# Kernel optimization log

Measured on AMD Instinct MI355X. Metric: run time of the kernel, lower is better.

Reference implementation:

```python
import jax, jax.numpy as jnp
import numpy as np


def _get_rel_pos(q_size, k_size, rel_pos):
    # table length is assumed == 2*max(q,k)-1 (no interpolation path)
    q_coords = jnp.arange(q_size)[:, None] * max(k_size / q_size, 1.0)
    k_coords = jnp.arange(k_size)[None, :] * max(q_size / k_size, 1.0)
    rel = (q_coords - k_coords + (k_size - 1) * max(q_size / k_size, 1.0)).astype(jnp.int32)
    return rel_pos[rel]  # (q_size, k_size, head_dim)


def setup_inputs() -> dict:
    key = jax.random.key(0)
    ks = jax.random.split(key, 7)
    B, N, C = 8, 1024, 768
    s = 0.02
    return {
        "x": jax.random.normal(ks[0], (B, N, C), jnp.float32),
        "qkv_w": jax.random.normal(ks[1], (3 * C, C), jnp.float32) * s,
        "qkv_b": jax.random.normal(ks[2], (3 * C,), jnp.float32) * s,
        "proj_w": jax.random.normal(ks[3], (C, C), jnp.float32) * s,
        "proj_b": jax.random.normal(ks[4], (C,), jnp.float32) * s,
        "rel_pos_h": jax.random.normal(ks[5], (63, 64), jnp.float32) * s,
        "rel_pos_w": jax.random.normal(ks[6], (63, 64), jnp.float32) * s,
        "H": 32,
        "W": 32,
    }


def reference(x, qkv_w, qkv_b, proj_w, proj_b, rel_pos_h, rel_pos_w, H, W):
    B, N, C = x.shape
    hd = rel_pos_h.shape[-1]
    nh = C // hd
    scale = hd ** -0.5

    qkv = (x @ qkv_w.T + qkv_b).reshape(B, N, 3, nh, hd)
    q, k, v = [qkv[:, :, i].transpose(0, 2, 1, 3) for i in range(3)]  # (B, nh, N, hd)

    # decomposed relative position bias on the last H*W query/key tokens (here all of them)
    Rh = _get_rel_pos(H, H, rel_pos_h)  # (H, H, hd)
    Rw = _get_rel_pos(W, W, rel_pos_w)  # (W, W, hd)
    r_q = q.reshape(B * nh, H, W, hd)
    rel_h = jnp.einsum("bhwc,hkc->bhwk", r_q, Rh)  # (B*nh, H, W, H)
    rel_w = jnp.einsum("bhwc,wkc->bhwk", r_q, Rw)  # (B*nh, H, W, W)
    bias = (rel_h[..., :, None] + rel_w[..., None, :]).reshape(B, nh, N, N)

    scores = jnp.einsum("bhqd,bhkd->bhqk", q * scale, k) + bias
    attn = jax.nn.softmax(scores, axis=-1)
    out = jnp.einsum("bhqk,bhkd->bhqd", attn, v)  # (B, nh, N, hd)
    out = out.transpose(0, 2, 1, 3).reshape(B, N, C)
    out = out @ proj_w.T + proj_b

    pre_kv = jnp.stack([k.reshape(B * nh, N, hd), v.reshape(B * nh, N, hd)])
    return out, pre_kv
```

## Files before the change

kernel.cpp:

```cpp
#include <hip/hip_runtime.h>
#include <hip/hip_bf16.h>
#include <stdint.h>

typedef __attribute__((ext_vector_type(8))) short bf16x8;
typedef __attribute__((ext_vector_type(4))) float f32x4;

#define LOG2E 1.4426950408889634f

__device__ __forceinline__ float exp2_fast(float x) {
  float r; asm("v_exp_f32 %0, %1" : "=v"(r) : "v"(x)); return r;
}

__device__ __forceinline__ void gload_lds16(const void* g, void* l) {
  typedef __attribute__((address_space(1))) void gv_t;
  typedef __attribute__((address_space(3))) void lv_t;
  __builtin_amdgcn_global_load_lds((gv_t*)(uintptr_t)g,
                                   (lv_t*)(uint32_t)(uintptr_t)l, 16, 0, 0);
}

__global__ __launch_bounds__(256) void cvt_bf16(const float* __restrict__ src,
                                                __hip_bfloat16* __restrict__ dst, int n4) {
  int i = blockIdx.x * 256 + threadIdx.x;
  if (i < n4) {
    float4 f = ((const float4*)src)[i];
    union { ushort4 u; __hip_bfloat16 h[4]; } pk;
    pk.h[0] = __float2bfloat16(f.x);
    pk.h[1] = __float2bfloat16(f.y);
    pk.h[2] = __float2bfloat16(f.z);
    pk.h[3] = __float2bfloat16(f.w);
    ((ushort4*)dst)[i] = pk.u;
  }
}

__global__ __launch_bounds__(256) void cvt_bf16_pad(const float* __restrict__ src,
                                                    __hip_bfloat16* __restrict__ dst,
                                                    int n4src, int n4tot, float scale) {
  int i = blockIdx.x * 256 + threadIdx.x;
  if (i < n4tot) {
    float4 f = (i < n4src) ? ((const float4*)src)[i] : make_float4(0.f, 0.f, 0.f, 0.f);
    union { ushort4 u; __hip_bfloat16 h[4]; } pk;
    pk.h[0] = __float2bfloat16(f.x * scale);
    pk.h[1] = __float2bfloat16(f.y * scale);
    pk.h[2] = __float2bfloat16(f.z * scale);
    pk.h[3] = __float2bfloat16(f.w * scale);
    ((ushort4*)dst)[i] = pk.u;
  }
}

__device__ __forceinline__ void gemm_tile_compute(const __hip_bfloat16* __restrict__ A,
                                                  const __hip_bfloat16* __restrict__ Bm,
                                                  int K, int bm, int bn,
                                                  f32x4 acc[4][4], char* lbase) {
  const int tid = threadIdx.x;
  const int lane = tid & 63, w = tid >> 6;
  const int wr = w >> 1, wc = w & 1;
  const int rrow = lane & 15, g16 = lane >> 4;

  for (int k0 = 0; k0 < K; k0 += 32) {
    #pragma unroll
    for (int i = 0; i < 2; ++i) {
      int c = i * 4 + w;
      int b = c * 1024 + (lane << 4);
      int row = b >> 6;
      int cbs = ((b >> 4) & 3) ^ (row & 3);
      const char* ga = (const char*)(A + (size_t)(bm * 128 + row) * K + k0) + cbs * 16;
      gload_lds16(ga, lbase + c * 1024);
      const char* gb = (const char*)(Bm + (size_t)(bn * 128 + row) * K + k0) + cbs * 16;
      gload_lds16(gb, lbase + 8192 + c * 1024);
    }
    asm volatile("s_waitcnt vmcnt(0)" ::: "memory");
    __syncthreads();

    bf16x8 af[4], bfr[4];
    #pragma unroll
    for (int i = 0; i < 4; ++i) {
      int row = wr * 64 + i * 16 + rrow;
      af[i] = *(const bf16x8*)(lbase + row * 64 + ((g16 * 16) ^ ((row & 3) << 4)));
      int col = wc * 64 + i * 16 + rrow;
      bfr[i] = *(const bf16x8*)(lbase + 8192 + col * 64 + ((g16 * 16) ^ ((col & 3) << 4)));
    }
    __builtin_amdgcn_s_setprio(1);
    #pragma unroll
    for (int i = 0; i < 4; ++i)
      #pragma unroll
      for (int j = 0; j < 4; ++j)
        acc[i][j] = __builtin_amdgcn_mfma_f32_16x16x32_bf16(af[i], bfr[j], acc[i][j], 0, 0, 0);
    __builtin_amdgcn_s_setprio(0);
    __syncthreads();
  }
}

__global__ __launch_bounds__(256) void gemm_qkv_kernel(
    const __hip_bfloat16* __restrict__ xb, const __hip_bfloat16* __restrict__ wqkv,
    const float* __restrict__ qkv_b,
    __hip_bfloat16* __restrict__ Qws, __hip_bfloat16* __restrict__ Kws,
    __hip_bfloat16* __restrict__ Vws, float* __restrict__ prekv) {
  __shared__ char smem[16384];
  f32x4 acc[4][4];
  const f32x4 z4 = {0.f, 0.f, 0.f, 0.f};
  #pragma unroll
  for (int i = 0; i < 4; ++i)
    #pragma unroll
    for (int j = 0; j < 4; ++j) acc[i][j] = z4;

  const int bn = blockIdx.x, bm = blockIdx.y;
  gemm_tile_compute(xb, wqkv, 768, bm, bn, acc, smem);

  const int lane = threadIdx.x & 63, w = threadIdx.x >> 6;
  const int wr = w >> 1, wc = w & 1;
  const int col0 = lane & 15, g = lane >> 4;
  #pragma unroll
  for (int j = 0; j < 4; ++j) {
    int n = bn * 128 + wc * 64 + j * 16 + col0;
    float bias = qkv_b[n];
    int which = n / 768;
    int head = (n >> 6) % 12;
    int d = n & 63;
    #pragma unroll
    for (int i = 0; i < 4; ++i) {
      #pragma unroll
      for (int r = 0; r < 4; ++r) {
        int m = bm * 128 + wr * 64 + i * 16 + g * 4 + r;
        float v = acc[i][j][r] + bias;
        int b = m >> 10, t = m & 1023;
        size_t idx = ((size_t)(b * 12 + head) << 16) + (t << 6) + d;
        __hip_bfloat16 hv = __float2bfloat16(v);
        if (which == 0) {
          Qws[idx] = hv;
        } else if (which == 1) {
          Kws[idx] = hv; prekv[idx] = v;
        } else {
          Vws[idx] = hv; prekv[6291456 + idx] = v;
        }
      }
    }
  }
}

__global__ __launch_bounds__(256) void gemm_proj_kernel(
    const __hip_bfloat16* __restrict__ Ows, const __hip_bfloat16* __restrict__ wproj,
    const float* __restrict__ proj_b, float* __restrict__ out) {
  __shared__ char smem[16384];
  f32x4 acc[4][4];
  const f32x4 z4 = {0.f, 0.f, 0.f, 0.f};
  #pragma unroll
  for (int i = 0; i < 4; ++i)
    #pragma unroll
    for (int j = 0; j < 4; ++j) acc[i][j] = z4;

  const int bn = blockIdx.x, bm = blockIdx.y;
  gemm_tile_compute(Ows, wproj, 768, bm, bn, acc, smem);

  const int lane = threadIdx.x & 63, w = threadIdx.x >> 6;
  const int wr = w >> 1, wc = w & 1;
  const int col0 = lane & 15, g = lane >> 4;
  #pragma unroll
  for (int j = 0; j < 4; ++j) {
    int n = bn * 128 + wc * 64 + j * 16 + col0;
    float bias = proj_b[n];
    #pragma unroll
    for (int i = 0; i < 4; ++i) {
      #pragma unroll
      for (int r = 0; r < 4; ++r) {
        int m = bm * 128 + wr * 64 + i * 16 + g * 4 + r;
        out[(size_t)m * 768 + n] = acc[i][j][r] + bias;
      }
    }
  }
}

#define VSWZ(hd) ((((hd) ^ ((hd) >> 3)) & 7) << 4)
__global__ __launch_bounds__(256, 3) void flash_attn(
    const __hip_bfloat16* __restrict__ Qws, const __hip_bfloat16* __restrict__ Kws,
    const __hip_bfloat16* __restrict__ Vws, const __hip_bfloat16* __restrict__ rphb,
    const __hip_bfloat16* __restrict__ rpwb, __hip_bfloat16* __restrict__ Ows) {
  __shared__ alignas(16) char smem[49152];
  float* s_relh = (float*)smem;
  char*  s_kt   = smem + 16384;
  char*  s_vt   = smem + 24576;
  char*  s_pt   = smem + 32768;
  float* s_rw   = (float*)(smem + 32768);

  const int tid = threadIdx.x, lane = tid & 63, w = tid >> 6;
  const int g16 = lane >> 4, c16 = lane & 15;
  const int bid = blockIdx.x;
  const int qt = bid / 96, bh = bid - qt * 96;
  const int q0 = qt * 128;
  const int b = bh / 12, head = bh - b * 12;
  const size_t bhbase = (size_t)bh << 16;

  bf16x8 qf[2][2];
  {
    const __hip_bfloat16* qp = Qws + bhbase + (size_t)(q0 + w * 32 + c16) * 64 + g16 * 8;
    qf[0][0] = *(const bf16x8*)qp;
    qf[0][1] = *(const bf16x8*)(qp + 32);
    qf[1][0] = *(const bf16x8*)(qp + 16 * 64);
    qf[1][1] = *(const bf16x8*)(qp + 16 * 64 + 32);
  }

  const f32x4 z4 = {0.f, 0.f, 0.f, 0.f};

  {
    f32x4 gh[2][4], gw[2][4];
    #pragma unroll
    for (int mb = 0; mb < 2; ++mb)
      #pragma unroll
      for (int nf = 0; nf < 4; ++nf) { gh[mb][nf] = z4; gw[mb][nf] = z4; }
    #pragma unroll
    for (int kc = 0; kc < 2; ++kc) {
      #pragma unroll
      for (int nf = 0; nf < 4; ++nf) {
        int j = nf * 16 + c16;
        bf16x8 th = *(const bf16x8*)(rphb + j * 64 + kc * 32 + g16 * 8);
        bf16x8 tw = *(const bf16x8*)(rpwb + j * 64 + kc * 32 + g16 * 8);
        gh[0][nf] = __builtin_amdgcn_mfma_f32_16x16x32_bf16(qf[0][kc], th, gh[0][nf], 0, 0, 0);
        gh[1][nf] = __builtin_amdgcn_mfma_f32_16x16x32_bf16(qf[1][kc], th, gh[1][nf], 0, 0, 0);
        gw[0][nf] = __builtin_amdgcn_mfma_f32_16x16x32_bf16(qf[0][kc], tw, gw[0][nf], 0, 0, 0);
        gw[1][nf] = __builtin_amdgcn_mfma_f32_16x16x32_bf16(qf[1][kc], tw, gw[1][nf], 0, 0, 0);
      }
    }
    const int hq = (q0 >> 5) + w;
    #pragma unroll
    for (int mb = 0; mb < 2; ++mb) {
      #pragma unroll
      for (int nf = 0; nf < 4; ++nf) {
        int j = nf * 16 + c16;
        int khh = hq - j + 31;
        #pragma unroll
        for (int r = 0; r < 4; ++r) {
          int rowin = mb * 16 + g16 * 4 + r;
          int lrow = w * 32 + rowin;
          if (khh >= 0 && khh < 32) s_relh[lrow * 32 + khh] = gh[mb][nf][r];
          int kww = rowin - j + 31;
          if (kww >= 0 && kww < 32) s_rw[lrow * 32 + kww] = gw[mb][nf][r];
        }
      }
    }
  }
  asm volatile("s_waitcnt lgkmcnt(0)" ::: "memory");
  float rw0[2][4], rw1[2][4];
  #pragma unroll
  for (int rb = 0; rb < 2; ++rb)
    #pragma unroll
    for (int r = 0; r < 4; ++r) {
      int lrow = w * 32 + rb * 16 + g16 * 4 + r;
      rw0[rb][r] = s_rw[lrow * 32 + c16];
      rw1[rb][r] = s_rw[lrow * 32 + 16 + c16];
    }

  f32x4 o[2][4];
  float m_r[2][4], l_r[2][4];
  #pragma unroll
  for (int rb = 0; rb < 2; ++rb) {
    #pragma unroll
    for (int hf = 0; hf < 4; ++hf) o[rb][hf] = z4;
    #pragma unroll
    for (int r = 0; r < 4; ++r) { m_r[rb][r] = -1e30f; l_r[rb][r] = 0.f; }
  }

  const float SCALE2 = 0.125f * LOG2E;
  const int kp = tid >> 3;
  const int hd0 = (tid & 7) * 8;

  for (int kt0 = 0; kt0 < 1024; kt0 += 64) {
    #pragma unroll
    for (int i = 0; i < 2; ++i) {
      int c = w * 2 + i;
      int row = c * 8 + (lane >> 3);
      int cbs = (lane & 7) ^ (row & 7);
      const char* g = (const char*)(Kws + bhbase + (size_t)(kt0 + row) * 64) + cbs * 16;
      gload_lds16(g, s_kt + c * 1024);
    }
    asm volatile("" ::: "memory");
    const __hip_bfloat16* vr = Vws + bhbase + (size_t)(kt0 + 2 * kp) * 64 + hd0;
    bf16x8 va = *(const bf16x8*)vr;
    bf16x8 vb = *(const bf16x8*)(vr + 64);
    asm volatile("s_waitcnt vmcnt(2)" ::: "memory");
    __builtin_amdgcn_s_barrier();

    f32x4 s[2][4];
    #pragma unroll
    for (int rb = 0; rb < 2; ++rb)
      #pragma unroll
      for (int kf = 0; kf < 4; ++kf) s[rb][kf] = z4;
    __builtin_amdgcn_s_setprio(1);
    #pragma unroll
    for (int kc = 0; kc < 2; ++kc) {
      #pragma unroll
      for (int kf = 0; kf < 4; ++kf) {
        int key = kf * 16 + c16;
        int byte = key * 128 + (((kc * 32 + g16 * 8) * 2) ^ ((key & 7) << 4));
        bf16x8 kfr = *(const bf16x8*)(s_kt + byte);
        s[0][kf] = __builtin_amdgcn_mfma_f32_16x16x32_bf16(qf[0][kc], kfr, s[0][kf], 0, 0, 0);
        s[1][kf] = __builtin_amdgcn_mfma_f32_16x16x32_bf16(qf[1][kc], kfr, s[1][kf], 0, 0, 0);
      }
    }
    __builtin_amdgcn_s_setprio(0);

    asm volatile("s_waitcnt vmcnt(0)" ::: "memory");
    #pragma unroll
    for (int j = 0; j < 8; ++j) {
      int hd = hd0 + j;
      union { ushort2 u2; uint32_t u; } pk;
      pk.u2.x = (unsigned short)va[j];
      pk.u2.y = (unsigned short)vb[j];
      *(uint32_t*)(s_vt + hd * 128 + ((4 * kp) ^ VSWZ(hd))) = pk.u;
    }

    int kh0 = kt0 >> 5;
    f32x4 facv[2];
    #pragma unroll
    for (int rb = 0; rb < 2; ++rb) {
      float rh0[4], rh1[4];
      #pragma unroll
      for (int r = 0; r < 4; ++r) {
        int lrow = w * 32 + rb * 16 + g16 * 4 + r;
        float2 rh = *(const float2*)&s_relh[lrow * 32 + kh0];
        rh0[r] = rh.x; rh1[r] = rh.y;
      }
      #pragma unroll
      for (int kf = 0; kf < 4; ++kf)
        #pragma unroll
        for (int r = 0; r < 4; ++r)
          s[rb][kf][r] = fmaf(s[rb][kf][r], SCALE2,
                              ((kf >> 1) ? rh1[r] : rh0[r]) +
                              ((kf & 1) ? rw1[rb][r] : rw0[rb][r]));
      #pragma unroll
      for (int r = 0; r < 4; ++r) {
        float tm = fmaxf(fmaxf(s[rb][0][r], s[rb][1][r]), fmaxf(s[rb][2][r], s[rb][3][r]));
        tm = fmaxf(tm, __shfl_xor(tm, 1));
        tm = fmaxf(tm, __shfl_xor(tm, 2));
        tm = fmaxf(tm, __shfl_xor(tm, 4));
        tm = fmaxf(tm, __shfl_xor(tm, 8));
        float mold = m_r[rb][r];
        float mnew = fmaxf(mold, tm);
        float fac = exp2_fast(mold - mnew);
        m_r[rb][r] = mnew;
        facv[rb][r] = fac;
        float psum = 0.f;
        #pragma unroll
        for (int kf = 0; kf < 4; ++kf) {
          float p = exp2_fast(s[rb][kf][r] - mnew);
          s[rb][kf][r] = p;
          psum += p;
        }
        psum += __shfl_xor(psum, 1);
        psum += __shfl_xor(psum, 2);
        psum += __shfl_xor(psum, 4);
        psum += __shfl_xor(psum, 8);
        l_r[rb][r] = fmaf(l_r[rb][r], fac, psum);
      }
    }
    bool nr = (facv[0][0] == 1.f) & (facv[0][1] == 1.f) & (facv[0][2] == 1.f) &
              (facv[0][3] == 1.f) & (facv[1][0] == 1.f) & (facv[1][1] == 1.f) &
              (facv[1][2] == 1.f) & (facv[1][3] == 1.f);
    if (!__all(nr)) {
      #pragma unroll
      for (int rb = 0; rb < 2; ++rb)
        #pragma unroll
        for (int hf = 0; hf < 4; ++hf) o[rb][hf] *= facv[rb];
    }

    #pragma unroll
    for (int rb = 0; rb < 2; ++rb)
      #pragma unroll
      for (int kf = 0; kf < 4; ++kf) {
        int key = kf * 16 + c16;
        #pragma unroll
        for (int r = 0; r < 4; ++r) {
          int prow = rb * 16 + g16 * 4 + r;
          int byte = w * 4096 + prow * 128 + ((key * 2) ^ ((prow & 7) << 4));
          *(__hip_bfloat16*)(s_pt + byte) = __float2bfloat16(s[rb][kf][r]);
        }
      }

    asm volatile("s_waitcnt lgkmcnt(0)" ::: "memory");
    __builtin_amdgcn_s_barrier();

    __builtin_amdgcn_s_setprio(1);
    #pragma unroll
    for (int kc = 0; kc < 2; ++kc) {
      bf16x8 pf[2];
      #pragma unroll
      for (int rb = 0; rb < 2; ++rb) {
        int prow = rb * 16 + c16;
        int byte = w * 4096 + prow * 128 + (((kc * 32 + g16 * 8) * 2) ^ ((prow & 7) << 4));
        pf[rb] = *(const bf16x8*)(s_pt + byte);
      }
      #pragma unroll
      for (int hf = 0; hf < 4; ++hf) {
        int hd = hf * 16 + c16;
        int byte = hd * 128 + (((kc * 32 + g16 * 8) * 2) ^ VSWZ(hd));
        bf16x8 vf = *(const bf16x8*)(s_vt + byte);
        o[0][hf] = __builtin_amdgcn_mfma_f32_16x16x32_bf16(pf[0], vf, o[0][hf], 0, 0, 0);
        o[1][hf] = __builtin_amdgcn_mfma_f32_16x16x32_bf16(pf[1], vf, o[1][hf], 0, 0, 0);
      }
    }
    __builtin_amdgcn_s_setprio(0);
  }

  #pragma unroll
  for (int rb = 0; rb < 2; ++rb) {
    #pragma unroll
    for (int r = 0; r < 4; ++r) {
      int row = q0 + w * 32 + rb * 16 + g16 * 4 + r;
      float inv = 1.0f / l_r[rb][r];
      size_t base = ((size_t)b * 1024 + row) * 768 + head * 64;
      #pragma unroll
      for (int hf = 0; hf < 4; ++hf)
        Ows[base + hf * 16 + c16] = __float2bfloat16(o[rb][hf][r] * inv);
    }
  }
}

extern "C" void kernel_launch(void* const* d_in, const int* in_sizes, int n_in,
                              void* d_out, int out_size, void* d_ws, size_t ws_size,
                              hipStream_t stream) {
  const float* x      = (const float*)d_in[0];
  const float* qkv_w  = (const float*)d_in[1];
  const float* qkv_b  = (const float*)d_in[2];
  const float* proj_w = (const float*)d_in[3];
  const float* proj_b = (const float*)d_in[4];
  const float* rph    = (const float*)d_in[5];
  const float* rpw    = (const float*)d_in[6];

  char* ws = (char*)d_ws;
  __hip_bfloat16* xb    = (__hip_bfloat16*)(ws);
  __hip_bfloat16* wqkv  = (__hip_bfloat16*)(ws + 12582912);
  __hip_bfloat16* wproj = (__hip_bfloat16*)(ws + 16121856);
  __hip_bfloat16* Qws   = (__hip_bfloat16*)(ws + 17301504);
  __hip_bfloat16* Kws   = (__hip_bfloat16*)(ws + 29884416);
  __hip_bfloat16* Vws   = (__hip_bfloat16*)(ws + 42467328);
  __hip_bfloat16* rphb  = (__hip_bfloat16*)(ws + 55050240);
  __hip_bfloat16* rpwb  = (__hip_bfloat16*)(ws + 55058432);
  __hip_bfloat16* Ows   = xb;

  float* out   = (float*)d_out;
  float* prekv = out + 6291456;

  cvt_bf16<<<6144, 256, 0, stream>>>(x, xb, 1572864);
  cvt_bf16<<<1728, 256, 0, stream>>>(qkv_w, wqkv, 442368);
  cvt_bf16<<<576, 256, 0, stream>>>(proj_w, wproj, 147456);
  cvt_bf16_pad<<<4, 256, 0, stream>>>(rph, rphb, 1008, 1024, LOG2E);
  cvt_bf16_pad<<<4, 256, 0, stream>>>(rpw, rpwb, 1008, 1024, LOG2E);
  gemm_qkv_kernel<<<dim3(18, 64), 256, 0, stream>>>(xb, wqkv, qkv_b, Qws, Kws, Vws, prekv);
  flash_attn<<<768, 256, 0, stream>>>(Qws, Kws, Vws, rphb, rpwb, Ows);
  gemm_proj_kernel<<<dim3(6, 64), 256, 0, stream>>>(Ows, wproj, proj_b, out);
}
```

Before: 367.2 us.

## Double-buffer K and V tiles in flash attention, store rel-h bias as bf16

Unrolls the key loop by two and double-buffers the K tile in LDS, while V is prefetched into registers one tile ahead. The aim is to overlap global loads with the current tile's MFMA and softmax work instead of waiting on each load before compute. To make room for the second K buffer, the rel-h bias table in LDS is stored as bf16 instead of fp32, which halves its size but loses some precision in the bias. The code also issues an extra wrap-around prefetch at the end of the loop and relies on careful vmcnt counts for correctness.

```diff
diff --git a/kernel.cpp b/kernel.cpp
--- a/kernel.cpp
+++ b/kernel.cpp
@@ -9,6 +9,12 @@
 
 __device__ __forceinline__ float exp2_fast(float x) {
   float r; asm("v_exp_f32 %0, %1" : "=v"(r) : "v"(x)); return r;
+}
+
+__device__ __forceinline__ float bf16bits_to_f32(unsigned short h) {
+  union { uint32_t u; float f; } c;
+  c.u = ((uint32_t)h) << 16;
+  return c.f;
 }
 
 __device__ __forceinline__ void gload_lds16(const void* g, void* l) {
@@ -170,13 +176,14 @@
 }
 
 #define VSWZ(hd) ((((hd) ^ ((hd) >> 3)) & 7) << 4)
+
 __global__ __launch_bounds__(256, 3) void flash_attn(
     const __hip_bfloat16* __restrict__ Qws, const __hip_bfloat16* __restrict__ Kws,
     const __hip_bfloat16* __restrict__ Vws, const __hip_bfloat16* __restrict__ rphb,
     const __hip_bfloat16* __restrict__ rpwb, __hip_bfloat16* __restrict__ Ows) {
   __shared__ alignas(16) char smem[49152];
-  float* s_relh = (float*)smem;
-  char*  s_kt   = smem + 16384;
+  char*  s_relh = smem;
+  char*  s_kt   = smem + 8192;
   char*  s_vt   = smem + 24576;
   char*  s_pt   = smem + 32768;
   float* s_rw   = (float*)(smem + 32768);
@@ -230,7 +237,8 @@
         for (int r = 0; r < 4; ++r) {
           int rowin = mb * 16 + g16 * 4 + r;
           int lrow = w * 32 + rowin;
-          if (khh >= 0 && khh < 32) s_relh[lrow * 32 + khh] = gh[mb][nf][r];
+          if (khh >= 0 && khh < 32)
+            *(__hip_bfloat16*)(s_relh + (lrow * 32 + khh) * 2) = __float2bfloat16(gh[mb][nf][r]);
           int kww = rowin - j + 31;
           if (kww >= 0 && kww < 32) s_rw[lrow * 32 + kww] = gw[mb][nf][r];
         }
@@ -262,142 +270,158 @@
   const int kp = tid >> 3;
   const int hd0 = (tid & 7) * 8;
 
-  for (int kt0 = 0; kt0 < 1024; kt0 += 64) {
-    #pragma unroll
-    for (int i = 0; i < 2; ++i) {
-      int c = w * 2 + i;
-      int row = c * 8 + (lane >> 3);
-      int cbs = (lane & 7) ^ (row & 7);
-      const char* g = (const char*)(Kws + bhbase + (size_t)(kt0 + row) * 64) + cbs * 16;
-      gload_lds16(g, s_kt + c * 1024);
-    }
-    asm volatile("" ::: "memory");
-    const __hip_bfloat16* vr = Vws + bhbase + (size_t)(kt0 + 2 * kp) * 64 + hd0;
-    bf16x8 va = *(const bf16x8*)vr;
-    bf16x8 vb = *(const bf16x8*)(vr + 64);
-    asm volatile("s_waitcnt vmcnt(2)" ::: "memory");
+#define ISSUE_K(kt, bufofs)                                                             \
+  {                                                                                     \
+    _Pragma("unroll")                                                                   \
+    for (int i = 0; i < 2; ++i) {                                                       \
+      int c = w * 2 + i;                                                                \
+      int row = c * 8 + (lane >> 3);                                                    \
+      int cbs = (lane & 7) ^ (row & 7);                                                 \
+      const char* g = (const char*)(Kws + bhbase + (size_t)((kt) + row) * 64) + cbs * 16; \
+      gload_lds16(g, s_kt + (bufofs) + c * 1024);                                       \
+    }                                                                                   \
+  }
+
+#define ISSUE_V(kt, va, vb)                                                             \
+  { const __hip_bfloat16* vr = Vws + bhbase + (size_t)((kt) + 2 * kp) * 64 + hd0;       \
+    va = *(const bf16x8*)vr; vb = *(const bf16x8*)(vr + 64); }
+
+#define TILE(kt0v, bufofs, va, vb)                                                      \
+  {                                                                                     \
+    f32x4 s[2][4];                                                                      \
+    _Pragma("unroll")                                                                   \
+    for (int rb = 0; rb < 2; ++rb)                                                      \
+      _Pragma("unroll")                                                                 \
+      for (int kf = 0; kf < 4; ++kf) s[rb][kf] = z4;                                    \
+    __builtin_amdgcn_s_setprio(1);                                                      \
+    _Pragma("unroll")                                                                   \
+    for (int kc = 0; kc < 2; ++kc) {                                                    \
+      _Pragma("unroll")                                                                 \
+      for (int kf = 0; kf < 4; ++kf) {                                                  \
+        int key = kf * 16 + c16;                                                        \
+        int byte = (bufofs) + key * 128 + (((kc * 32 + g16 * 8) * 2) ^ ((key & 7) << 4)); \
+        bf16x8 kfr = *(const bf16x8*)(s_kt + byte);                                     \
+        s[0][kf] = __builtin_amdgcn_mfma_f32_16x16x32_bf16(qf[0][kc], kfr, s[0][kf], 0, 0, 0); \
+        s[1][kf] = __builtin_amdgcn_mfma_f32_16x16x32_bf16(qf[1][kc], kfr, s[1][kf], 0, 0, 0); \
+      }                                                                                 \
+    }                                                                                   \
+    __builtin_amdgcn_s_setprio(0);                                                      \
+    _Pragma("unroll")                                                                   \
+    for (int j = 0; j < 8; ++j) {                                                       \
+      int hd = hd0 + j;                                                                 \
+      union { ushort2 u2; uint32_t u; } pk;                                             \
+      pk.u2.x = (unsigned short)va[j];                                                  \
+      pk.u2.y = (unsigned short)vb[j];                                                  \
+      *(uint32_t*)(s_vt + hd * 128 + ((4 * kp) ^ VSWZ(hd))) = pk.u;                     \
+    }                                                                                   \
+    int kh0 = (kt0v) >> 5;                                                              \
+    f32x4 facv[2];                                                                      \
+    _Pragma("unroll")                                                                   \
+    for (int rb = 0; rb < 2; ++rb) {                                                    \
+      float rh0[4], rh1[4];                                                             \
+      _Pragma("unroll")                                                                 \
+      for (int r = 0; r < 4; ++r) {                                                     \
+        int lrow = w * 32 + rb * 16 + g16 * 4 + r;                                      \
+        uint32_t rhu = *(const uint32_t*)(s_relh + (lrow * 32 + kh0) * 2);              \
+        rh0[r] = bf16bits_to_f32((unsigned short)(rhu & 0xffff));                       \
+        rh1[r] = bf16bits_to_f32((unsigned short)(rhu >> 16));                          \
+      }                                                                                 \
+      _Pragma("unroll")                                                                 \
+      for (int kf = 0; kf < 4; ++kf)                                                    \
+        _Pragma("unroll")                                                               \
+        for (int r = 0; r < 4; ++r)                                                     \
+          s[rb][kf][r] = fmaf(s[rb][kf][r], SCALE2,                                     \
+                              ((kf >> 1) ? rh1[r] : rh0[r]) +                           \
+                              ((kf & 1) ? rw1[rb][r] : rw0[rb][r]));                    \
+      _Pragma("unroll")                                                                 \
+      for (int r = 0; r < 4; ++r) {                                                     \
+        float tm = fmaxf(fmaxf(s[rb][0][r], s[rb][1][r]), fmaxf(s[rb][2][r], s[rb][3][r])); \
+        tm = fmaxf(tm, __shfl_xor(tm, 1));                                              \
+        tm = fmaxf(tm, __shfl_xor(tm, 2));                                              \
+        tm = fmaxf(tm, __shfl_xor(tm, 4));                                              \
+        tm = fmaxf(tm, __shfl_xor(tm, 8));                                              \
+        float mold = m_r[rb][r];                                                        \
+        float mnew = fmaxf(mold, tm);                                                   \
+        float fac = exp2_fast(mold - mnew);                                             \
+        m_r[rb][r] = mnew;                                                              \
+        facv[rb][r] = fac;                                                              \
+        float psum = 0.f;                                                               \
+        _Pragma("unroll")                                                               \
+        for (int kf = 0; kf < 4; ++kf) {                                                \
+          float p = exp2_fast(s[rb][kf][r] - mnew);                                     \
+          s[rb][kf][r] = p;                                                             \
+          psum += p;                                                                    \
+        }                                                                               \
+        psum += __shfl_xor(psum, 1);                                                    \
+        psum += __shfl_xor(psum, 2);                                                    \
+        psum += __shfl_xor(psum, 4);                                                    \
+        psum += __shfl_xor(psum, 8);                                                    \
+        l_r[rb][r] = fmaf(l_r[rb][r], fac, psum);                                       \
+      }                                                                                 \
+    }                                                                                   \
+    bool nr = (facv[0][0] == 1.f) & (facv[0][1] == 1.f) & (facv[0][2] == 1.f) &         \
+              (facv[0][3] == 1.f) & (facv[1][0] == 1.f) & (facv[1][1] == 1.f) &         \
+              (facv[1][2] == 1.f) & (facv[1][3] == 1.f);                                \
+    if (!__all(nr)) {                                                                   \
+      _Pragma("unroll")                                                                 \
+      for (int rb = 0; rb < 2; ++rb)                                                    \
+        _Pragma("unroll")                                                               \
+        for (int hf = 0; hf < 4; ++hf) o[rb][hf] *= facv[rb];                           \
+    }                                                                                   \
+    _Pragma("unroll")                                                                   \
+    for (int rb = 0; rb < 2; ++rb)                                                      \
+      _Pragma("unroll")                                                                 \
+      for (int kf = 0; kf < 4; ++kf) {                                                  \
+        int key = kf * 16 + c16;                                                        \
+        _Pragma("unroll")                                                               \
+        for (int r = 0; r < 4; ++r) {                                                   \
+          int prow = rb * 16 + g16 * 4 + r;                                             \
+          int byte = w * 4096 + prow * 128 + ((key * 2) ^ ((prow & 7) << 4));           \
+          *(__hip_bfloat16*)(s_pt + byte) = __float2bfloat16(s[rb][kf][r]);             \
+        }                                                                               \
+      }                                                                                 \
+    asm volatile("s_waitcnt lgkmcnt(0)" ::: "memory");                                  \
+    __builtin_amdgcn_s_barrier();                                                       \
+    __builtin_amdgcn_s_setprio(1);                                                      \
+    _Pragma("unroll")                                                                   \
+    for (int kc = 0; kc < 2; ++kc) {                                                    \
+      bf16x8 pf[2];                                                                     \
+      _Pragma("unroll")                                                                 \
+      for (int rb = 0; rb < 2; ++rb) {                                                  \
+        int prow = rb * 16 + c16;                                                       \
+        int byte = w * 4096 + prow * 128 + (((kc * 32 + g16 * 8) * 2) ^ ((prow & 7) << 4)); \
+        pf[rb] = *(const bf16x8*)(s_pt + byte);                                         \
+      }                                                                                 \
+      _Pragma("unroll")                                                                 \
+      for (int hf = 0; hf < 4; ++hf) {                                                  \
+        int hd = hf * 16 + c16;                                                         \
+        int byte = hd * 128 + (((kc * 32 + g16 * 8) * 2) ^ VSWZ(hd));                   \
+        bf16x8 vf = *(const bf16x8*)(s_vt + byte);                                      \
+        o[0][hf] = __builtin_amdgcn_mfma_f32_16x16x32_bf16(pf[0], vf, o[0][hf], 0, 0, 0); \
+        o[1][hf] = __builtin_amdgcn_mfma_f32_16x16x32_bf16(pf[1], vf, o[1][hf], 0, 0, 0); \
+      }                                                                                 \
+    }                                                                                   \
+    __builtin_amdgcn_s_setprio(0);                                                      \
+  }
+
+  bf16x8 vaA, vbA, vaB, vbB;
+  ISSUE_K(0, 0);
+  ISSUE_V(0, vaA, vbA);
+
+  for (int it = 0; it < 8; ++it) {
+    int t0 = it * 128;
+    ISSUE_K((t0 + 64) & 1023, 8192);
+    ISSUE_V((t0 + 64) & 1023, vaB, vbB);
+    asm volatile("s_waitcnt vmcnt(4)" ::: "memory");
     __builtin_amdgcn_s_barrier();
-
-    f32x4 s[2][4];
-    #pragma unroll
-    for (int rb = 0; rb < 2; ++rb)
-      #pragma unroll
-      for (int kf = 0; kf < 4; ++kf) s[rb][kf] = z4;
-    __builtin_amdgcn_s_setprio(1);
-    #pragma unroll
-    for (int kc = 0; kc < 2; ++kc) {
-      #pragma unroll
-      for (int kf = 0; kf < 4; ++kf) {
-        int key = kf * 16 + c16;
-        int byte = key * 128 + (((kc * 32 + g16 * 8) * 2) ^ ((key & 7) << 4));
-        bf16x8 kfr = *(const bf16x8*)(s_kt + byte);
-        s[0][kf] = __builtin_amdgcn_mfma_f32_16x16x32_bf16(qf[0][kc], kfr, s[0][kf], 0, 0, 0);
-        s[1][kf] = __builtin_amdgcn_mfma_f32_16x16x32_bf16(qf[1][kc], kfr, s[1][kf], 0, 0, 0);
-      }
-    }
-    __builtin_amdgcn_s_setprio(0);
-
-    asm volatile("s_waitcnt vmcnt(0)" ::: "memory");
-    #pragma unroll
-    for (int j = 0; j < 8; ++j) {
-      int hd = hd0 + j;
-      union { ushort2 u2; uint32_t u; } pk;
-      pk.u2.x = (unsigned short)va[j];
-      pk.u2.y = (unsigned short)vb[j];
-      *(uint32_t*)(s_vt + hd * 128 + ((4 * kp) ^ VSWZ(hd))) = pk.u;
-    }
-
-    int kh0 = kt0 >> 5;
-    f32x4 facv[2];
-    #pragma unroll
-    for (int rb = 0; rb < 2; ++rb) {
-      float rh0[4], rh1[4];
-      #pragma unroll
-      for (int r = 0; r < 4; ++r) {
-        int lrow = w * 32 + rb * 16 + g16 * 4 + r;
-        float2 rh = *(const float2*)&s_relh[lrow * 32 + kh0];
-        rh0[r] = rh.x; rh1[r] = rh.y;
-      }
-      #pragma unroll
-      for (int kf = 0; kf < 4; ++kf)
-        #pragma unroll
-        for (int r = 0; r < 4; ++r)
-          s[rb][kf][r] = fmaf(s[rb][kf][r], SCALE2,
-                              ((kf >> 1) ? rh1[r] : rh0[r]) +
-                              ((kf & 1) ? rw1[rb][r] : rw0[rb][r]));
-      #pragma unroll
-      for (int r = 0; r < 4; ++r) {
-        float tm = fmaxf(fmaxf(s[rb][0][r], s[rb][1][r]), fmaxf(s[rb][2][r], s[rb][3][r]));
-        tm = fmaxf(tm, __shfl_xor(tm, 1));
-        tm = fmaxf(tm, __shfl_xor(tm, 2));
-        tm = fmaxf(tm, __shfl_xor(tm, 4));
-        tm = fmaxf(tm, __shfl_xor(tm, 8));
-        float mold = m_r[rb][r];
-        float mnew = fmaxf(mold, tm);
-        float fac = exp2_fast(mold - mnew);
-        m_r[rb][r] = mnew;
-        facv[rb][r] = fac;
-        float psum = 0.f;
-        #pragma unroll
-        for (int kf = 0; kf < 4; ++kf) {
-          float p = exp2_fast(s[rb][kf][r] - mnew);
-          s[rb][kf][r] = p;
-          psum += p;
-        }
-        psum += __shfl_xor(psum, 1);
-        psum += __shfl_xor(psum, 2);
-        psum += __shfl_xor(psum, 4);
-        psum += __shfl_xor(psum, 8);
-        l_r[rb][r] = fmaf(l_r[rb][r], fac, psum);
-      }
-    }
-    bool nr = (facv[0][0] == 1.f) & (facv[0][1] == 1.f) & (facv[0][2] == 1.f) &
-              (facv[0][3] == 1.f) & (facv[1][0] == 1.f) & (facv[1][1] == 1.f) &
-              (facv[1][2] == 1.f) & (facv[1][3] == 1.f);
-    if (!__all(nr)) {
-      #pragma unroll
-      for (int rb = 0; rb < 2; ++rb)
-        #pragma unroll
-        for (int hf = 0; hf < 4; ++hf) o[rb][hf] *= facv[rb];
-    }
-
-    #pragma unroll
-    for (int rb = 0; rb < 2; ++rb)
-      #pragma unroll
-      for (int kf = 0; kf < 4; ++kf) {
-        int key = kf * 16 + c16;
-        #pragma unroll
-        for (int r = 0; r < 4; ++r) {
-          int prow = rb * 16 + g16 * 4 + r;
-          int byte = w * 4096 + prow * 128 + ((key * 2) ^ ((prow & 7) << 4));
-          *(__hip_bfloat16*)(s_pt + byte) = __float2bfloat16(s[rb][kf][r]);
-        }
-      }
-
-    asm volatile("s_waitcnt lgkmcnt(0)" ::: "memory");
+    TILE(t0, 0, vaA, vbA);
+    ISSUE_K((t0 + 128) & 1023, 0);
+    ISSUE_V((t0 + 128) & 1023, vaA, vbA);
+    asm volatile("s_waitcnt vmcnt(4)" ::: "memory");
     __builtin_amdgcn_s_barrier();
-
-    __builtin_amdgcn_s_setprio(1);
-    #pragma unroll
-    for (int kc = 0; kc < 2; ++kc) {
-      bf16x8 pf[2];
-      #pragma unroll
-      for (int rb = 0; rb < 2; ++rb) {
-        int prow = rb * 16 + c16;
-        int byte = w * 4096 + prow * 128 + (((kc * 32 + g16 * 8) * 2) ^ ((prow & 7) << 4));
-        pf[rb] = *(const bf16x8*)(s_pt + byte);
-      }
-      #pragma unroll
-      for (int hf = 0; hf < 4; ++hf) {
-        int hd = hf * 16 + c16;
-        int byte = hd * 128 + (((kc * 32 + g16 * 8) * 2) ^ VSWZ(hd));
-        bf16x8 vf = *(const bf16x8*)(s_vt + byte);
-        o[0][hf] = __builtin_amdgcn_mfma_f32_16x16x32_bf16(pf[0], vf, o[0][hf], 0, 0, 0);
-        o[1][hf] = __builtin_amdgcn_mfma_f32_16x16x32_bf16(pf[1], vf, o[1][hf], 0, 0, 0);
-      }
-    }
-    __builtin_amdgcn_s_setprio(0);
-  }
+    TILE(t0 + 64, 8192, vaB, vbB);
+  }
+  asm volatile("s_waitcnt vmcnt(0)" ::: "memory");
 
   #pragma unroll
   for (int rb = 0; rb < 2; ++rb) {
@@ -411,6 +435,9 @@
         Ows[base + hf * 16 + c16] = __float2bfloat16(o[rb][hf][r] * inv);
     }
   }
+#undef ISSUE_K
+#undef ISSUE_V
+#undef TILE
 }
 
 extern "C" void kernel_launch(void* const* d_in, const int* in_sizes, int n_in,
```

Result: slower. 474.0 us (+29.1%).

## Double-buffer K tile loads in flash attention and store rel_h bias as bf16

Applied to the files above, without the earlier changes.

Prefetches the next K tile into a second LDS buffer while the current tile is consumed, so global-to-LDS latency overlaps with the MFMA work. To free LDS for the second buffer, the rel_h bias table is stored in bf16 instead of fp32 and widened on read. The occupancy hint in launch_bounds is removed. The bf16 bias loses precision. The wrap-around prefetch on the last iteration loads a tile that is never used.

```diff
diff --git a/kernel.cpp b/kernel.cpp
--- a/kernel.cpp
+++ b/kernel.cpp
@@ -9,6 +9,12 @@
 
 __device__ __forceinline__ float exp2_fast(float x) {
   float r; asm("v_exp_f32 %0, %1" : "=v"(r) : "v"(x)); return r;
+}
+
+__device__ __forceinline__ float bf16bits_to_f32(unsigned short h) {
+  union { uint32_t u; float f; } c;
+  c.u = ((uint32_t)h) << 16;
+  return c.f;
 }
 
 __device__ __forceinline__ void gload_lds16(const void* g, void* l) {
@@ -170,13 +176,14 @@
 }
 
 #define VSWZ(hd) ((((hd) ^ ((hd) >> 3)) & 7) << 4)
-__global__ __launch_bounds__(256, 3) void flash_attn(
+
+__global__ __launch_bounds__(256) void flash_attn(
     const __hip_bfloat16* __restrict__ Qws, const __hip_bfloat16* __restrict__ Kws,
     const __hip_bfloat16* __restrict__ Vws, const __hip_bfloat16* __restrict__ rphb,
     const __hip_bfloat16* __restrict__ rpwb, __hip_bfloat16* __restrict__ Ows) {
   __shared__ alignas(16) char smem[49152];
-  float* s_relh = (float*)smem;
-  char*  s_kt   = smem + 16384;
+  char*  s_relh = smem;
+  char*  s_kt   = smem + 8192;
   char*  s_vt   = smem + 24576;
   char*  s_pt   = smem + 32768;
   float* s_rw   = (float*)(smem + 32768);
@@ -230,7 +237,8 @@
         for (int r = 0; r < 4; ++r) {
           int rowin = mb * 16 + g16 * 4 + r;
           int lrow = w * 32 + rowin;
-          if (khh >= 0 && khh < 32) s_relh[lrow * 32 + khh] = gh[mb][nf][r];
+          if (khh >= 0 && khh < 32)
+            *(__hip_bfloat16*)(s_relh + (lrow * 32 + khh) * 2) = __float2bfloat16(gh[mb][nf][r]);
           int kww = rowin - j + 31;
           if (kww >= 0 && kww < 32) s_rw[lrow * 32 + kww] = gw[mb][nf][r];
         }
@@ -261,21 +269,32 @@
   const float SCALE2 = 0.125f * LOG2E;
   const int kp = tid >> 3;
   const int hd0 = (tid & 7) * 8;
-
-  for (int kt0 = 0; kt0 < 1024; kt0 += 64) {
-    #pragma unroll
-    for (int i = 0; i < 2; ++i) {
-      int c = w * 2 + i;
-      int row = c * 8 + (lane >> 3);
-      int cbs = (lane & 7) ^ (row & 7);
-      const char* g = (const char*)(Kws + bhbase + (size_t)(kt0 + row) * 64) + cbs * 16;
-      gload_lds16(g, s_kt + c * 1024);
-    }
-    asm volatile("" ::: "memory");
+  const int krow = (w * 2) * 8 + (lane >> 3);
+  const int krow2 = (w * 2 + 1) * 8 + (lane >> 3);
+  const int kcbs = ((lane & 7) ^ (krow & 7)) * 16;
+  const int kcbs2 = ((lane & 7) ^ (krow2 & 7)) * 16;
+
+  gload_lds16((const char*)(Kws + bhbase + (size_t)krow * 64) + kcbs,
+              s_kt + (w * 2) * 1024);
+  gload_lds16((const char*)(Kws + bhbase + (size_t)krow2 * 64) + kcbs2,
+              s_kt + (w * 2 + 1) * 1024);
+
+  for (int t = 0; t < 16; ++t) {
+    const int kt0 = t << 6;
+    const int bo = (t & 1) << 13;
+    const int bn = ((t + 1) & 1) << 13;
     const __hip_bfloat16* vr = Vws + bhbase + (size_t)(kt0 + 2 * kp) * 64 + hd0;
     bf16x8 va = *(const bf16x8*)vr;
     bf16x8 vb = *(const bf16x8*)(vr + 64);
-    asm volatile("s_waitcnt vmcnt(2)" ::: "memory");
+    asm volatile("" ::: "memory");
+    {
+      const int ktn = (kt0 + 64) & 1023;
+      gload_lds16((const char*)(Kws + bhbase + (size_t)(ktn + krow) * 64) + kcbs,
+                  s_kt + bn + (w * 2) * 1024);
+      gload_lds16((const char*)(Kws + bhbase + (size_t)(ktn + krow2) * 64) + kcbs2,
+                  s_kt + bn + (w * 2 + 1) * 1024);
+    }
+    asm volatile("s_waitcnt vmcnt(4)" ::: "memory");
     __builtin_amdgcn_s_barrier();
 
     f32x4 s[2][4];
@@ -289,7 +308,7 @@
       #pragma unroll
       for (int kf = 0; kf < 4; ++kf) {
         int key = kf * 16 + c16;
-        int byte = key * 128 + (((kc * 32 + g16 * 8) * 2) ^ ((key & 7) << 4));
+        int byte = bo + key * 128 + (((kc * 32 + g16 * 8) * 2) ^ ((key & 7) << 4));
         bf16x8 kfr = *(const bf16x8*)(s_kt + byte);
         s[0][kf] = __builtin_amdgcn_mfma_f32_16x16x32_bf16(qf[0][kc], kfr, s[0][kf], 0, 0, 0);
         s[1][kf] = __builtin_amdgcn_mfma_f32_16x16x32_bf16(qf[1][kc], kfr, s[1][kf], 0, 0, 0);
@@ -297,7 +316,7 @@
     }
     __builtin_amdgcn_s_setprio(0);
 
-    asm volatile("s_waitcnt vmcnt(0)" ::: "memory");
+    asm volatile("s_waitcnt vmcnt(2)" ::: "memory");
     #pragma unroll
     for (int j = 0; j < 8; ++j) {
       int hd = hd0 + j;
@@ -315,8 +334,9 @@
       #pragma unroll
       for (int r = 0; r < 4; ++r) {
         int lrow = w * 32 + rb * 16 + g16 * 4 + r;
-        float2 rh = *(const float2*)&s_relh[lrow * 32 + kh0];
-        rh0[r] = rh.x; rh1[r] = rh.y;
+        uint32_t rhu = *(const uint32_t*)(s_relh + (lrow * 32 + kh0) * 2);
+        rh0[r] = bf16bits_to_f32((unsigned short)(rhu & 0xffff));
+        rh1[r] = bf16bits_to_f32((unsigned short)(rhu >> 16));
       }
       #pragma unroll
       for (int kf = 0; kf < 4; ++kf)
@@ -398,6 +418,7 @@
     }
     __builtin_amdgcn_s_setprio(0);
   }
+  asm volatile("s_waitcnt vmcnt(0)" ::: "memory");
 
   #pragma unroll
   for (int rb = 0; rb < 2; ++rb) {
```

Result: faster. 345.4 us (-5.9%).
